# Optimization experiments

Hardware: AMD Instinct MI355X
Metric: run time of the kernel (lower is better)

## Reference

```python
import jax, jax.numpy as jnp
import numpy as np

N, K, M, C, OUT, S = 80000, 8, 1000, 128, 64, 2
EPS = 1e-5


def _bn(x, g, b, m, v):
    # eval-mode BatchNorm1d applied over the last (channel) axis
    return (x - m) * (g / jnp.sqrt(v + EPS)) + b


def setup_inputs() -> dict:
    key = jax.random.key(0)
    ks = jax.random.split(key, 40)
    it = iter(range(40))
    rn = lambda sh, s=1.0: jax.random.normal(ks[next(it)], sh, dtype=jnp.float32) * s
    ru = lambda sh: jax.random.uniform(ks[next(it)], sh, dtype=jnp.float32, minval=0.5, maxval=1.5)
    w = 0.05
    inp = {}
    inp["sp_fea"] = rn((M, C))
    inp["sp_xyz"] = rn((M, 3))
    inp["o_p_fea"] = rn((N, C))
    inp["p_xyz"] = rn((N, 3))
    # linear_q / linear_k / linear_v  (in_planes -> mid_planes)
    inp["Wq"] = rn((C, C), w); inp["bq"] = jnp.zeros((C,), jnp.float32)
    inp["Wk"] = rn((C, C), w); inp["bk"] = jnp.zeros((C,), jnp.float32)
    inp["Wv"] = rn((C, C), w); inp["bv"] = jnp.zeros((C,), jnp.float32)
    # linear_p: Linear(3,3) -> BN(3) -> ReLU -> Linear(3, mid)
    inp["Wp1"] = rn((3, 3), 0.5); inp["bp1"] = jnp.zeros((3,), jnp.float32)
    inp["gp"] = 1.0 + rn((3,), 0.1); inp["betap"] = rn((3,), 0.1)
    inp["mp"] = rn((3,), 0.1); inp["vp"] = ru((3,))
    inp["Wp2"] = rn((3, C), 0.3); inp["bp2"] = jnp.zeros((C,), jnp.float32)
    # linear_w: BN(mid) -> ReLU -> Linear(mid,out) -> BN(out) -> ReLU -> Linear(out,out)
    inp["g1"] = 1.0 + rn((C,), 0.1); inp["beta1"] = rn((C,), 0.1)
    inp["m1"] = rn((C,), 0.1); inp["v1"] = ru((C,))
    inp["W1"] = rn((C, OUT), w); inp["b1"] = jnp.zeros((OUT,), jnp.float32)
    inp["g2"] = 1.0 + rn((OUT,), 0.1); inp["beta2"] = rn((OUT,), 0.1)
    inp["m2"] = rn((OUT,), 0.1); inp["v2"] = ru((OUT,))
    inp["W2"] = rn((OUT, OUT), w); inp["b2"] = jnp.zeros((OUT,), jnp.float32)
    # index / offset inputs (ints)
    inp["c2p_idx_abs"] = jax.random.randint(ks[next(it)], (N, K), 0, M)
    inp["c2p_idx"] = jax.random.randint(ks[next(it)], (N, K), 0, M)
    inp["cluster_idx"] = jax.random.randint(ks[next(it)], (N,), 0, M)
    inp["offset"] = jnp.array([N], dtype=jnp.int32)
    inp["sp_offset"] = jnp.array([M], dtype=jnp.int32)
    return inp


def reference(sp_fea, sp_xyz, o_p_fea, p_xyz,
              Wq, bq, Wk, bk, Wv, bv,
              Wp1, bp1, gp, betap, mp, vp, Wp2, bp2,
              g1, beta1, m1, v1, W1, b1,
              g2, beta2, m2, v2, W2, b2,
              c2p_idx_abs, c2p_idx, cluster_idx, offset, sp_offset):
    q = o_p_fea @ Wq + bq                               # [N, C]
    k_sp = (sp_fea @ Wk + bk)[c2p_idx_abs]              # gather -> [N, K, C]
    v_sp = (sp_fea @ Wv + bv)[c2p_idx_abs]              # [N, K, C]
    p_e = sp_xyz[c2p_idx_abs]                           # [N, K, 3]
    # positional encoding MLP
    p_e = jax.nn.relu(_bn(p_e @ Wp1 + bp1, gp, betap, mp, vp)) @ Wp2 + bp2  # [N, K, C]
    # vector attention scores
    w = k_sp - q[:, None, :] + p_e                      # [N, K, C]
    w = jax.nn.relu(_bn(w, g1, beta1, m1, v1)) @ W1 + b1
    w = jax.nn.relu(_bn(w, g2, beta2, m2, v2)) @ W2 + b2  # [N, K, OUT]
    w = jax.nn.softmax(w, axis=1)                        # softmax over the K neighbors
    # shared-plane weighted sum
    bi = ((v_sp + p_e).reshape(N, K, S, C // S) * w[:, :, None, :]).reshape(N, K, C)
    bi = bi.sum(axis=2)                                  # [N, K]
    return jax.nn.softmax(bi, axis=1)                    # association matrix [N, K]
```

## Files before the change

kernel.cpp:

```cpp
#include <hip/hip_runtime.h>
#include <stdint.h>

#define EPS 1e-5f

#define NPTS 80000
#define CDIM 128
#define ODIM 64
#define KNBR 8
#define MSUP 1000

#define KP2H_OFF 0
#define UT_OFF   (256*1024)
#define WQF_OFF  (512*1024)
#define W1F_OFF  (544*1024)
#define W2F_OFF  (560*1024)
#define C1_OFF   (568*1024)
#define QSG_OFF  (576*1024)
#define WSTAGE_BYTES (16*1024 + 8*1024 + 256)

typedef float f32x4 __attribute__((ext_vector_type(4)));
typedef short bf16x8 __attribute__((ext_vector_type(8)));

union FragU { bf16x8 v; unsigned u[4]; uint4 q; };

#if __has_builtin(__builtin_amdgcn_cvt_pk_bf16_f32)
typedef __bf16 bf16x2_t __attribute__((ext_vector_type(2)));
#define HAVE_PK_BF16 1
#endif

__device__ inline unsigned pk_bf16(float lo, float hi) {
#ifdef HAVE_PK_BF16
  return __builtin_bit_cast(unsigned, __builtin_amdgcn_cvt_pk_bf16_f32(lo, hi));
#else
  unsigned a = __builtin_bit_cast(unsigned, lo);
  unsigned b = __builtin_bit_cast(unsigned, hi);
  a += 0x7FFFu + ((a >> 16) & 1u);
  b += 0x7FFFu + ((b >> 16) & 1u);
  return (a >> 16) | (b & 0xFFFF0000u);
#endif
}

__device__ inline void unpk(unsigned p, float& lo, float& hi) {
  lo = __builtin_bit_cast(float, p << 16);
  hi = __builtin_bit_cast(float, p & 0xFFFF0000u);
}

__global__ __launch_bounds__(256)
void k_prep(const float* __restrict__ sp_fea, const float* __restrict__ sp_xyz,
            const float* __restrict__ Wk, const float* __restrict__ bk,
            const float* __restrict__ Wv, const float* __restrict__ bv,
            const float* __restrict__ Wp1, const float* __restrict__ bp1,
            const float* __restrict__ gp, const float* __restrict__ betap,
            const float* __restrict__ mp, const float* __restrict__ vp,
            const float* __restrict__ Wp2, const float* __restrict__ bp2,
            const float* __restrict__ g1, const float* __restrict__ beta1,
            const float* __restrict__ m1, const float* __restrict__ v1,
            const float* __restrict__ bq,
            const float* __restrict__ Wq, const float* __restrict__ W1,
            const float* __restrict__ W2,
            const float* __restrict__ g2, const float* __restrict__ v2,
            const float* __restrict__ b1, const float* __restrict__ m2,
            const float* __restrict__ beta2, char* __restrict__ ws)
{
  if (blockIdx.x < 1000) {
    unsigned short* kp2h = (unsigned short*)(ws + KP2H_OFF);
    float* uT = (float*)(ws + UT_OFF);
    const int m = blockIdx.x;
    const int t = threadIdx.x;
    const int c = t & 127, half = t >> 7;
    __shared__ float fea[128];
    __shared__ float pk[128], pv[128];
    if (t < 128) fea[t] = sp_fea[m * 128 + t];
    __syncthreads();
    float kv = 0.f, vv = 0.f;
    const float* wkc = Wk + half * 64 * 128 + c;
    const float* wvc = Wv + half * 64 * 128 + c;
    const float* feah = fea + half * 64;
    #pragma unroll 8
    for (int d = 0; d < 64; ++d) {
      const float f = feah[d];
      kv = fmaf(f, wkc[d * 128], kv);
      vv = fmaf(f, wvc[d * 128], vv);
    }
    if (half) { pk[c] = kv; pv[c] = vv; }
    __syncthreads();
    if (!half) {
      kv += pk[c] + bk[c];
      vv += pv[c] + bv[c];
      const float x0 = sp_xyz[m*3+0], x1 = sp_xyz[m*3+1], x2 = sp_xyz[m*3+2];
      float pe = bp2[c];
      #pragma unroll
      for (int ii = 0; ii < 3; ++ii) {
        float s = bp1[ii] + x0*Wp1[0*3+ii] + x1*Wp1[1*3+ii] + x2*Wp1[2*3+ii];
        s = (s - mp[ii]) * (gp[ii] * rsqrtf(vp[ii] + EPS)) + betap[ii];
        s = fmaxf(s, 0.0f);
        pe += s * Wp2[ii*128 + c];
      }
      const float s1c = g1[c] * rsqrtf(v1[c] + EPS);
      const float kpv = (kv + pe - m1[c] - bq[c]) * s1c + beta1[c];
      kp2h[m*128 + c] = (unsigned short)(pk_bf16(kpv, kpv) & 0xFFFFu);
      pv[c] = vv + pe;
    }
    __syncthreads();
    if (t < 64) uT[m*64 + t] = pv[t] + pv[t + 64];
  } else {
    const int tid = (blockIdx.x - 1000) * 256 + threadIdx.x;
    if (tid < 2048) {
      const int e = tid, f = e >> 6, l = e & 63;
      const int kt = f >> 3, mt = f & 7;
      const int c = mt*16 + (l & 15);
      const int d0 = kt*32 + (l >> 4)*8;
      const float sc = g1[c] * rsqrtf(v1[c] + EPS);
      uint4 u;
      u.x = pk_bf16(Wq[(d0+0)*128 + c]*sc, Wq[(d0+1)*128 + c]*sc);
      u.y = pk_bf16(Wq[(d0+2)*128 + c]*sc, Wq[(d0+3)*128 + c]*sc);
      u.z = pk_bf16(Wq[(d0+4)*128 + c]*sc, Wq[(d0+5)*128 + c]*sc);
      u.w = pk_bf16(Wq[(d0+6)*128 + c]*sc, Wq[(d0+7)*128 + c]*sc);
      *(uint4*)(ws + WQF_OFF + e*16) = u;
    } else if (tid < 3072) {
      const int e = tid - 2048, f = e >> 6, l = e & 63;
      const int kt = f >> 2, jt = f & 3;
      const int j = jt*16 + (l & 15);
      const int c0 = kt*32 + (l >> 4)*8;
      const float sc = g2[j] * rsqrtf(v2[j] + EPS);
      uint4 u;
      u.x = pk_bf16(W1[(c0+0)*64 + j]*sc, W1[(c0+1)*64 + j]*sc);
      u.y = pk_bf16(W1[(c0+2)*64 + j]*sc, W1[(c0+3)*64 + j]*sc);
      u.z = pk_bf16(W1[(c0+4)*64 + j]*sc, W1[(c0+5)*64 + j]*sc);
      u.w = pk_bf16(W1[(c0+6)*64 + j]*sc, W1[(c0+7)*64 + j]*sc);
      *(uint4*)(ws + W1F_OFF + e*16) = u;
    } else if (tid < 3584) {
      const int e = tid - 3072, f = e >> 6, l = e & 63;
      const int kt2 = f >> 2, nt = f & 3;
      const int jp = nt*16 + (l & 15);
      const int j0 = kt2*32 + (l >> 4)*8;
      uint4 u;
      u.x = pk_bf16(W2[(j0+0)*64 + jp], W2[(j0+1)*64 + jp]);
      u.y = pk_bf16(W2[(j0+2)*64 + jp], W2[(j0+3)*64 + jp]);
      u.z = pk_bf16(W2[(j0+4)*64 + jp], W2[(j0+5)*64 + jp]);
      u.w = pk_bf16(W2[(j0+6)*64 + jp], W2[(j0+7)*64 + jp]);
      *(uint4*)(ws + W2F_OFF + e*16) = u;
    } else if (tid < 3648) {
      const int j = tid - 3584;
      const float sc = g2[j] * rsqrtf(v2[j] + EPS);
      ((float*)(ws + C1_OFF))[j] = (b1[j] - m2[j]) * sc + beta2[j];
    }
  }
}

__global__ __launch_bounds__(256, 4)
void k_q(const float* __restrict__ o_p_fea, char* __restrict__ ws)
{
  const bf16x8* wqf = (const bf16x8*)(ws + WQF_OFF);
  char* qs_g = ws + QSG_OFF;
  const int t = threadIdx.x;
  const int wave = t >> 6, l = t & 63;
  const int quad = l >> 4, row = l & 15;
  const int n0 = (blockIdx.x * 4 + wave) * 16;

  f32x4 qa[8];
  #pragma unroll
  for (int mt = 0; mt < 8; ++mt) qa[mt] = (f32x4){0.f, 0.f, 0.f, 0.f};
  const float* feab = o_p_fea + (size_t)(n0 + row) * 128;
  #pragma unroll
  for (int kt = 0; kt < 4; ++kt) {
    f32x4 fa = *(const f32x4*)(feab + kt*32 + quad*8);
    f32x4 fb = *(const f32x4*)(feab + kt*32 + quad*8 + 4);
    FragU bu;
    bu.u[0] = pk_bf16(fa[0], fa[1]);
    bu.u[1] = pk_bf16(fa[2], fa[3]);
    bu.u[2] = pk_bf16(fb[0], fb[1]);
    bu.u[3] = pk_bf16(fb[2], fb[3]);
    #pragma unroll
    for (int mt = 0; mt < 8; ++mt)
      qa[mt] = __builtin_amdgcn_mfma_f32_16x16x32_bf16(wqf[(kt*8+mt)*64 + l], bu.v, qa[mt], 0, 0, 0);
  }
  #pragma unroll
  for (int mt = 0; mt < 8; ++mt) {
    uint2 pp;
    pp.x = pk_bf16(qa[mt][0], qa[mt][1]);
    pp.y = pk_bf16(qa[mt][2], qa[mt][3]);
    *(uint2*)(qs_g + (size_t)(n0 + row) * 256 + mt*32 + quad*8) = pp;
  }
}

#define H2_PITCH 144
#define H2_SIZE  (16*144)
#define W1L_OFF  0
#define W2L_OFF  (16*1024)
#define C1L_OFF  (24*1024)
#define H2_BASE  24832
#define LDS_TOTAL (H2_BASE + 4*H2_SIZE)

__global__ __launch_bounds__(256, 3)
void k_main(const int* __restrict__ idx, const float* __restrict__ b2,
            const char* __restrict__ ws, float* __restrict__ out)
{
  const unsigned short* kp2h = (const unsigned short*)(ws + KP2H_OFF);
  const float* uT = (const float*)(ws + UT_OFF);
  const char* qs_g = ws + QSG_OFF;

  __shared__ __align__(16) char lds[LDS_TOTAL];
  const int t = threadIdx.x;
  const int wave = t >> 6, l = t & 63;
  const int quad = l >> 4, row = l & 15;
  char* h2_w = lds + H2_BASE + wave * H2_SIZE;

  const int sg = blockIdx.x * 4 + wave;
  const int n0 = sg * 16;
  const int idx_base = n0 * 8;
  const int nloc = row >> 3;

  {
    const uint4* src = (const uint4*)(ws + W1F_OFF);
    uint4* dst = (uint4*)lds;
    #pragma unroll
    for (int i = 0; i < 7; ++i) {
      const int e = t + i * 256;
      if (e < WSTAGE_BYTES / 16) dst[e] = src[e];
    }
  }

  int mr8[8];
  #pragma unroll
  for (int g = 0; g < 8; ++g) mr8[g] = idx[idx_base + g*16 + row];

  __syncthreads();

  f32x4 c1r[4];
  #pragma unroll
  for (int jt = 0; jt < 4; ++jt)
    c1r[jt] = *(const f32x4*)(lds + C1L_OFF + (jt*16 + quad*4)*4);
  float b2r[4];
  #pragma unroll
  for (int nt = 0; nt < 4; ++nt) b2r[nt] = b2[row + nt*16];

  int msc[4];
  #pragma unroll
  for (int rg = 0; rg < 4; ++rg) msc[rg] = idx[idx_base + quad*4 + rg];
  uint4 kfc[4], qpc[4];
  {
    const uint4* kr = (const uint4*)(kp2h + (size_t)mr8[0] * 128);
    const uint4* qr = (const uint4*)(qs_g + (size_t)(n0 + nloc) * 256);
    #pragma unroll
    for (int kt = 0; kt < 4; ++kt) { kfc[kt] = kr[kt*4 + quad]; qpc[kt] = qr[kt*4 + quad]; }
  }

  #pragma unroll 1
  for (int g = 0; g < 8; ++g) {
    int msn[4];
    uint4 kfn[4], qpn[4];
    if (g < 7) {
      #pragma unroll
      for (int rg = 0; rg < 4; ++rg) msn[rg] = idx[idx_base + (g+1)*16 + quad*4 + rg];
      const uint4* kr = (const uint4*)(kp2h + (size_t)mr8[g+1] * 128);
      const uint4* qr = (const uint4*)(qs_g + (size_t)(n0 + (g+1)*2 + nloc) * 256);
      #pragma unroll
      for (int kt = 0; kt < 4; ++kt) { kfn[kt] = kr[kt*4 + quad]; qpn[kt] = qr[kt*4 + quad]; }
    }
    float u4[4][4];
    #pragma unroll
    for (int rg = 0; rg < 4; ++rg) {
      const float* ur = uT + (size_t)msc[rg] * 64 + row;
      #pragma unroll
      for (int nt = 0; nt < 4; ++nt) u4[rg][nt] = ur[nt*16];
    }

    f32x4 a1[4];
    #pragma unroll
    for (int jt = 0; jt < 4; ++jt) a1[jt] = (f32x4){0.f, 0.f, 0.f, 0.f};
    #pragma unroll
    for (int kt = 0; kt < 4; ++kt) {
      const uint4 kp = kfc[kt];
      const uint4 qp = qpc[kt];
      FragU xf;
      {
        float klo, khi, qlo, qhi;
        unpk(kp.x, klo, khi); unpk(qp.x, qlo, qhi);
        xf.u[0] = pk_bf16(fmaxf(klo - qlo, 0.f), fmaxf(khi - qhi, 0.f));
        unpk(kp.y, klo, khi); unpk(qp.y, qlo, qhi);
        xf.u[1] = pk_bf16(fmaxf(klo - qlo, 0.f), fmaxf(khi - qhi, 0.f));
        unpk(kp.z, klo, khi); unpk(qp.z, qlo, qhi);
        xf.u[2] = pk_bf16(fmaxf(klo - qlo, 0.f), fmaxf(khi - qhi, 0.f));
        unpk(kp.w, klo, khi); unpk(qp.w, qlo, qhi);
        xf.u[3] = pk_bf16(fmaxf(klo - qlo, 0.f), fmaxf(khi - qhi, 0.f));
      }
      #pragma unroll
      for (int jt = 0; jt < 4; ++jt) {
        const bf16x8 wf = *(const bf16x8*)(lds + W1L_OFF + (kt*4+jt)*1024 + l*16);
        a1[jt] = __builtin_amdgcn_mfma_f32_16x16x32_bf16(wf, xf.v, a1[jt], 0, 0, 0);
      }
    }

    #pragma unroll
    for (int jt = 0; jt < 4; ++jt) {
      f32x4 v = a1[jt] + c1r[jt];
      uint2 pp;
      pp.x = pk_bf16(fmaxf(v[0], 0.f), fmaxf(v[1], 0.f));
      pp.y = pk_bf16(fmaxf(v[2], 0.f), fmaxf(v[3], 0.f));
      *(uint2*)(h2_w + row*H2_PITCH + (jt*16 + quad*4)*2) = pp;
    }

    f32x4 a2[4];
    #pragma unroll
    for (int nt = 0; nt < 4; ++nt) a2[nt] = (f32x4){0.f, 0.f, 0.f, 0.f};
    #pragma unroll
    for (int kt2 = 0; kt2 < 2; ++kt2) {
      const bf16x8 af = *(const bf16x8*)(h2_w + row*H2_PITCH + kt2*64 + quad*16);
      #pragma unroll
      for (int nt = 0; nt < 4; ++nt) {
        const bf16x8 wf = *(const bf16x8*)(lds + W2L_OFF + (kt2*4+nt)*1024 + l*16);
        a2[nt] = __builtin_amdgcn_mfma_f32_16x16x32_bf16(af, wf, a2[nt], 0, 0, 0);
      }
    }
    float e[4][4], rs[4];
    #pragma unroll
    for (int nt = 0; nt < 4; ++nt) {
      #pragma unroll
      for (int rg = 0; rg < 4; ++rg) e[nt][rg] = __expf(a2[nt][rg] + b2r[nt]);
      float s = e[nt][0] + e[nt][1] + e[nt][2] + e[nt][3];
      s += __shfl_xor(s, 16);
      rs[nt] = __builtin_amdgcn_rcpf(s);
    }
    float bi[4] = {0.f, 0.f, 0.f, 0.f};
    #pragma unroll
    for (int rg = 0; rg < 4; ++rg) {
      #pragma unroll
      for (int nt = 0; nt < 4; ++nt)
        bi[rg] = fmaf(e[nt][rg] * rs[nt], u4[rg][nt], bi[rg]);
    }
    #pragma unroll
    for (int rg = 0; rg < 4; ++rg) {
      float b = bi[rg];
      b += __shfl_xor(b, 1);
      b += __shfl_xor(b, 2);
      b += __shfl_xor(b, 4);
      b += __shfl_xor(b, 8);
      bi[rg] = b;
    }
    const float eb0 = __expf(bi[0]), eb1 = __expf(bi[1]);
    const float eb2 = __expf(bi[2]), eb3 = __expf(bi[3]);
    float sb = eb0 + eb1 + eb2 + eb3;
    sb += __shfl_xor(sb, 16);
    const float rsb = __builtin_amdgcn_rcpf(sb);
    if (row < 4) {
      const float vsel = row == 0 ? eb0 : row == 1 ? eb1 : row == 2 ? eb2 : eb3;
      out[n0*8 + g*16 + quad*4 + row] = vsel * rsb;
    }
    if (g < 7) {
      #pragma unroll
      for (int rg = 0; rg < 4; ++rg) msc[rg] = msn[rg];
      #pragma unroll
      for (int kt = 0; kt < 4; ++kt) { kfc[kt] = kfn[kt]; qpc[kt] = qpn[kt]; }
    }
  }
}

extern "C" void kernel_launch(void* const* d_in, const int* in_sizes, int n_in,
                              void* d_out, int out_size, void* d_ws, size_t ws_size,
                              hipStream_t stream)
{
  const float* sp_fea  = (const float*)d_in[0];
  const float* sp_xyz  = (const float*)d_in[1];
  const float* o_p_fea = (const float*)d_in[2];
  const float* Wq    = (const float*)d_in[4];
  const float* bq    = (const float*)d_in[5];
  const float* Wk    = (const float*)d_in[6];
  const float* bk    = (const float*)d_in[7];
  const float* Wv    = (const float*)d_in[8];
  const float* bv    = (const float*)d_in[9];
  const float* Wp1   = (const float*)d_in[10];
  const float* bp1   = (const float*)d_in[11];
  const float* gp    = (const float*)d_in[12];
  const float* betap = (const float*)d_in[13];
  const float* mp    = (const float*)d_in[14];
  const float* vp    = (const float*)d_in[15];
  const float* Wp2   = (const float*)d_in[16];
  const float* bp2   = (const float*)d_in[17];
  const float* g1    = (const float*)d_in[18];
  const float* beta1 = (const float*)d_in[19];
  const float* m1    = (const float*)d_in[20];
  const float* v1    = (const float*)d_in[21];
  const float* W1    = (const float*)d_in[22];
  const float* b1    = (const float*)d_in[23];
  const float* g2    = (const float*)d_in[24];
  const float* beta2 = (const float*)d_in[25];
  const float* m2    = (const float*)d_in[26];
  const float* v2    = (const float*)d_in[27];
  const float* W2    = (const float*)d_in[28];
  const float* b2    = (const float*)d_in[29];
  const int* c2p_idx_abs = (const int*)d_in[30];

  char* ws = (char*)d_ws;
  float* out = (float*)d_out;

  hipLaunchKernelGGL(k_prep, dim3(1015), dim3(256), 0, stream,
                     sp_fea, sp_xyz, Wk, bk, Wv, bv, Wp1, bp1, gp, betap, mp, vp,
                     Wp2, bp2, g1, beta1, m1, v1, bq,
                     Wq, W1, W2, g2, v2, b1, m2, beta2, ws);
  hipLaunchKernelGGL(k_q, dim3(1250), dim3(256), 0, stream,
                     o_p_fea, ws);
  hipLaunchKernelGGL(k_main, dim3(1250), dim3(256), 0, stream,
                     c2p_idx_abs, b2, ws, out);
}
```

Before: 221.5 us.

## Software-pipeline softmax epilogue one group behind MFMA and use packed bf16 ops

The exp/softmax/weighted-sum epilogue for each group now runs one iteration late, after the next group's MFMAs have been issued, so the transcendental and shuffle work can overlap matrix work. The separate unpack-to-fp32, subtract, relu and repack steps are replaced with native bf16 vector subtract and max, and the relu after layer 1 is done on packed bf16. Launch bounds go from 3 to 4 blocks per CU. The carried epilogue state adds register pressure against the tighter occupancy target, and subtracting in bf16 instead of fp32 changes rounding slightly.

Measured after the change: 414.5 us. 87.1% more time.

```diff
diff --git a/kernel.cpp b/kernel.cpp
--- a/kernel.cpp
+++ b/kernel.cpp
@@ -20,16 +20,18 @@
 
 typedef float f32x4 __attribute__((ext_vector_type(4)));
 typedef short bf16x8 __attribute__((ext_vector_type(8)));
+typedef __bf16 bf16v8 __attribute__((ext_vector_type(8)));
+typedef __bf16 bf16v4 __attribute__((ext_vector_type(4)));
 
 union FragU { bf16x8 v; unsigned u[4]; uint4 q; };
 
 #if __has_builtin(__builtin_amdgcn_cvt_pk_bf16_f32)
-typedef __bf16 bf16x2_t __attribute__((ext_vector_type(2)));
 #define HAVE_PK_BF16 1
 #endif
 
 __device__ inline unsigned pk_bf16(float lo, float hi) {
 #ifdef HAVE_PK_BF16
+  typedef __bf16 bf16x2_t __attribute__((ext_vector_type(2)));
   return __builtin_bit_cast(unsigned, __builtin_amdgcn_cvt_pk_bf16_f32(lo, hi));
 #else
   unsigned a = __builtin_bit_cast(unsigned, lo);
@@ -38,11 +40,6 @@
   b += 0x7FFFu + ((b >> 16) & 1u);
   return (a >> 16) | (b & 0xFFFF0000u);
 #endif
-}
-
-__device__ inline void unpk(unsigned p, float& lo, float& hi) {
-  lo = __builtin_bit_cast(float, p << 16);
-  hi = __builtin_bit_cast(float, p & 0xFFFF0000u);
 }
 
 __global__ __launch_bounds__(256)
@@ -192,7 +189,50 @@
 #define H2_BASE  24832
 #define LDS_TOTAL (H2_BASE + 4*H2_SIZE)
 
-__global__ __launch_bounds__(256, 3)
+struct EpiState { f32x4 a2[4]; float u4[4][4]; };
+
+__device__ __forceinline__ void epilogue(const EpiState& st, const float* b2r,
+                                         int quad, int row,
+                                         float* __restrict__ out, int base,
+                                         bool wr)
+{
+  float e[4][4], rs[4];
+  #pragma unroll
+  for (int nt = 0; nt < 4; ++nt) {
+    #pragma unroll
+    for (int rg = 0; rg < 4; ++rg) e[nt][rg] = __expf(st.a2[nt][rg] + b2r[nt]);
+    float s = e[nt][0] + e[nt][1] + e[nt][2] + e[nt][3];
+    s += __shfl_xor(s, 16);
+    rs[nt] = __builtin_amdgcn_rcpf(s);
+  }
+  float bi[4] = {0.f, 0.f, 0.f, 0.f};
+  #pragma unroll
+  for (int rg = 0; rg < 4; ++rg) {
+    #pragma unroll
+    for (int nt = 0; nt < 4; ++nt)
+      bi[rg] = fmaf(e[nt][rg] * rs[nt], st.u4[rg][nt], bi[rg]);
+  }
+  #pragma unroll
+  for (int rg = 0; rg < 4; ++rg) {
+    float b = bi[rg];
+    b += __shfl_xor(b, 1);
+    b += __shfl_xor(b, 2);
+    b += __shfl_xor(b, 4);
+    b += __shfl_xor(b, 8);
+    bi[rg] = b;
+  }
+  const float eb0 = __expf(bi[0]), eb1 = __expf(bi[1]);
+  const float eb2 = __expf(bi[2]), eb3 = __expf(bi[3]);
+  float sb = eb0 + eb1 + eb2 + eb3;
+  sb += __shfl_xor(sb, 16);
+  const float rsb = __builtin_amdgcn_rcpf(sb);
+  if (wr && row < 4) {
+    const float vsel = row == 0 ? eb0 : row == 1 ? eb1 : row == 2 ? eb2 : eb3;
+    out[base + quad*4 + row] = vsel * rsb;
+  }
+}
+
+__global__ __launch_bounds__(256, 4)
 void k_main(const int* __restrict__ idx, const float* __restrict__ b2,
             const char* __restrict__ ws, float* __restrict__ out)
 {
@@ -246,6 +286,14 @@
     for (int kt = 0; kt < 4; ++kt) { kfc[kt] = kr[kt*4 + quad]; qpc[kt] = qr[kt*4 + quad]; }
   }
 
+  EpiState st;
+  #pragma unroll
+  for (int nt = 0; nt < 4; ++nt) {
+    st.a2[nt] = (f32x4){0.f, 0.f, 0.f, 0.f};
+    #pragma unroll
+    for (int rg = 0; rg < 4; ++rg) st.u4[nt][rg] = 0.f;
+  }
+
   #pragma unroll 1
   for (int g = 0; g < 8; ++g) {
     int msn[4];
@@ -258,12 +306,12 @@
       #pragma unroll
       for (int kt = 0; kt < 4; ++kt) { kfn[kt] = kr[kt*4 + quad]; qpn[kt] = qr[kt*4 + quad]; }
     }
-    float u4[4][4];
+    float u4n[4][4];
     #pragma unroll
     for (int rg = 0; rg < 4; ++rg) {
       const float* ur = uT + (size_t)msc[rg] * 64 + row;
       #pragma unroll
-      for (int nt = 0; nt < 4; ++nt) u4[rg][nt] = ur[nt*16];
+      for (int nt = 0; nt < 4; ++nt) u4n[rg][nt] = ur[nt*16];
     }
 
     f32x4 a1[4];
@@ -271,20 +319,12 @@
     for (int jt = 0; jt < 4; ++jt) a1[jt] = (f32x4){0.f, 0.f, 0.f, 0.f};
     #pragma unroll
     for (int kt = 0; kt < 4; ++kt) {
-      const uint4 kp = kfc[kt];
-      const uint4 qp = qpc[kt];
+      const bf16v8 kv = __builtin_bit_cast(bf16v8, kfc[kt]);
+      const bf16v8 qv = __builtin_bit_cast(bf16v8, qpc[kt]);
+      bf16v8 z = {};
+      bf16v8 x = __builtin_elementwise_max((bf16v8)(kv - qv), z);
       FragU xf;
-      {
-        float klo, khi, qlo, qhi;
-        unpk(kp.x, klo, khi); unpk(qp.x, qlo, qhi);
-        xf.u[0] = pk_bf16(fmaxf(klo - qlo, 0.f), fmaxf(khi - qhi, 0.f));
-        unpk(kp.y, klo, khi); unpk(qp.y, qlo, qhi);
-        xf.u[1] = pk_bf16(fmaxf(klo - qlo, 0.f), fmaxf(khi - qhi, 0.f));
-        unpk(kp.z, klo, khi); unpk(qp.z, qlo, qhi);
-        xf.u[2] = pk_bf16(fmaxf(klo - qlo, 0.f), fmaxf(khi - qhi, 0.f));
-        unpk(kp.w, klo, khi); unpk(qp.w, qlo, qhi);
-        xf.u[3] = pk_bf16(fmaxf(klo - qlo, 0.f), fmaxf(khi - qhi, 0.f));
-      }
+      xf.q = __builtin_bit_cast(uint4, x);
       #pragma unroll
       for (int jt = 0; jt < 4; ++jt) {
         const bf16x8 wf = *(const bf16x8*)(lds + W1L_OFF + (kt*4+jt)*1024 + l*16);
@@ -296,8 +336,12 @@
     for (int jt = 0; jt < 4; ++jt) {
       f32x4 v = a1[jt] + c1r[jt];
       uint2 pp;
-      pp.x = pk_bf16(fmaxf(v[0], 0.f), fmaxf(v[1], 0.f));
-      pp.y = pk_bf16(fmaxf(v[2], 0.f), fmaxf(v[3], 0.f));
+      pp.x = pk_bf16(v[0], v[1]);
+      pp.y = pk_bf16(v[2], v[3]);
+      bf16v4 h = __builtin_bit_cast(bf16v4, pp);
+      bf16v4 z4 = {};
+      h = __builtin_elementwise_max(h, z4);
+      pp = __builtin_bit_cast(uint2, h);
       *(uint2*)(h2_w + row*H2_PITCH + (jt*16 + quad*4)*2) = pp;
     }
 
@@ -313,40 +357,19 @@
         a2[nt] = __builtin_amdgcn_mfma_f32_16x16x32_bf16(af, wf, a2[nt], 0, 0, 0);
       }
     }
-    float e[4][4], rs[4];
-    #pragma unroll
-    for (int nt = 0; nt < 4; ++nt) {
-      #pragma unroll
-      for (int rg = 0; rg < 4; ++rg) e[nt][rg] = __expf(a2[nt][rg] + b2r[nt]);
-      float s = e[nt][0] + e[nt][1] + e[nt][2] + e[nt][3];
-      s += __shfl_xor(s, 16);
-      rs[nt] = __builtin_amdgcn_rcpf(s);
-    }
-    float bi[4] = {0.f, 0.f, 0.f, 0.f};
-    #pragma unroll
-    for (int rg = 0; rg < 4; ++rg) {
-      #pragma unroll
-      for (int nt = 0; nt < 4; ++nt)
-        bi[rg] = fmaf(e[nt][rg] * rs[nt], u4[rg][nt], bi[rg]);
-    }
-    #pragma unroll
-    for (int rg = 0; rg < 4; ++rg) {
-      float b = bi[rg];
-      b += __shfl_xor(b, 1);
-      b += __shfl_xor(b, 2);
-      b += __shfl_xor(b, 4);
-      b += __shfl_xor(b, 8);
-      bi[rg] = b;
-    }
-    const float eb0 = __expf(bi[0]), eb1 = __expf(bi[1]);
-    const float eb2 = __expf(bi[2]), eb3 = __expf(bi[3]);
-    float sb = eb0 + eb1 + eb2 + eb3;
-    sb += __shfl_xor(sb, 16);
-    const float rsb = __builtin_amdgcn_rcpf(sb);
-    if (row < 4) {
-      const float vsel = row == 0 ? eb0 : row == 1 ? eb1 : row == 2 ? eb2 : eb3;
-      out[n0*8 + g*16 + quad*4 + row] = vsel * rsb;
-    }
+
+    {
+      const int gm1 = g - 1;
+      const int base = n0*8 + (gm1 < 0 ? 0 : gm1)*16;
+      epilogue(st, b2r, quad, row, out, base, gm1 >= 0);
+    }
+
+    #pragma unroll
+    for (int nt = 0; nt < 4; ++nt) st.a2[nt] = a2[nt];
+    #pragma unroll
+    for (int rg = 0; rg < 4; ++rg)
+      #pragma unroll
+      for (int nt = 0; nt < 4; ++nt) st.u4[rg][nt] = u4n[rg][nt];
     if (g < 7) {
       #pragma unroll
       for (int rg = 0; rg < 4; ++rg) msc[rg] = msn[rg];
@@ -354,6 +377,7 @@
       for (int kt = 0; kt < 4; ++kt) { kfc[kt] = kfn[kt]; qpc[kt] = qpn[kt]; }
     }
   }
+  epilogue(st, b2r, quad, row, out, n0*8 + 7*16, true);
 }
 
 extern "C" void kernel_launch(void* const* d_in, const int* in_sizes, int n_in,
```

## Stage Wq fragments in LDS and use packed bf16 subtract/max ops

Applied to the files above, without the earlier changes.

The q-projection kernel now copies the 32KB pre-fragmented Wq block into shared memory once per workgroup and reads MFMA A-fragments from LDS instead of global memory. In the main attention kernel, the k-q subtraction and ReLU are done directly on bf16 vectors instead of unpacking to fp32 and repacking, and the post-GEMM ReLU is applied after packing to bf16. The goal is fewer global loads and fewer ALU conversion instructions. In exchange it adds 32KB LDS per block in k_q, which can lower occupancy, and doing the subtraction in bf16 rounds differently. Packed bf16 arithmetic may also not map to native instructions, in which case the compiler expands it.

New measurement: 213.7 us. 1.04x faster.

```diff
diff --git a/kernel.cpp b/kernel.cpp
--- a/kernel.cpp
+++ b/kernel.cpp
@@ -20,16 +20,18 @@
 
 typedef float f32x4 __attribute__((ext_vector_type(4)));
 typedef short bf16x8 __attribute__((ext_vector_type(8)));
+typedef __bf16 bf16v8 __attribute__((ext_vector_type(8)));
+typedef __bf16 bf16v4 __attribute__((ext_vector_type(4)));
 
 union FragU { bf16x8 v; unsigned u[4]; uint4 q; };
 
 #if __has_builtin(__builtin_amdgcn_cvt_pk_bf16_f32)
-typedef __bf16 bf16x2_t __attribute__((ext_vector_type(2)));
 #define HAVE_PK_BF16 1
 #endif
 
 __device__ inline unsigned pk_bf16(float lo, float hi) {
 #ifdef HAVE_PK_BF16
+  typedef __bf16 bf16x2_t __attribute__((ext_vector_type(2)));
   return __builtin_bit_cast(unsigned, __builtin_amdgcn_cvt_pk_bf16_f32(lo, hi));
 #else
   unsigned a = __builtin_bit_cast(unsigned, lo);
@@ -38,11 +40,6 @@
   b += 0x7FFFu + ((b >> 16) & 1u);
   return (a >> 16) | (b & 0xFFFF0000u);
 #endif
-}
-
-__device__ inline void unpk(unsigned p, float& lo, float& hi) {
-  lo = __builtin_bit_cast(float, p << 16);
-  hi = __builtin_bit_cast(float, p & 0xFFFF0000u);
 }
 
 __global__ __launch_bounds__(256)
@@ -151,12 +148,20 @@
 __global__ __launch_bounds__(256, 4)
 void k_q(const float* __restrict__ o_p_fea, char* __restrict__ ws)
 {
-  const bf16x8* wqf = (const bf16x8*)(ws + WQF_OFF);
+  __shared__ __align__(16) char ldsq[32*1024];
   char* qs_g = ws + QSG_OFF;
   const int t = threadIdx.x;
   const int wave = t >> 6, l = t & 63;
   const int quad = l >> 4, row = l & 15;
   const int n0 = (blockIdx.x * 4 + wave) * 16;
+
+  {
+    const uint4* src = (const uint4*)(ws + WQF_OFF);
+    uint4* dst = (uint4*)ldsq;
+    #pragma unroll
+    for (int i = 0; i < 8; ++i) dst[t + i*256] = src[t + i*256];
+  }
+  __syncthreads();
 
   f32x4 qa[8];
   #pragma unroll
@@ -172,8 +177,10 @@
     bu.u[2] = pk_bf16(fb[0], fb[1]);
     bu.u[3] = pk_bf16(fb[2], fb[3]);
     #pragma unroll
-    for (int mt = 0; mt < 8; ++mt)
-      qa[mt] = __builtin_amdgcn_mfma_f32_16x16x32_bf16(wqf[(kt*8+mt)*64 + l], bu.v, qa[mt], 0, 0, 0);
+    for (int mt = 0; mt < 8; ++mt) {
+      const bf16x8 wf = *(const bf16x8*)(ldsq + ((kt*8+mt)*64 + l)*16);
+      qa[mt] = __builtin_amdgcn_mfma_f32_16x16x32_bf16(wf, bu.v, qa[mt], 0, 0, 0);
+    }
   }
   #pragma unroll
   for (int mt = 0; mt < 8; ++mt) {
@@ -271,20 +278,12 @@
     for (int jt = 0; jt < 4; ++jt) a1[jt] = (f32x4){0.f, 0.f, 0.f, 0.f};
     #pragma unroll
     for (int kt = 0; kt < 4; ++kt) {
-      const uint4 kp = kfc[kt];
-      const uint4 qp = qpc[kt];
+      const bf16v8 kv = __builtin_bit_cast(bf16v8, kfc[kt]);
+      const bf16v8 qv = __builtin_bit_cast(bf16v8, qpc[kt]);
+      bf16v8 z = {};
+      bf16v8 x = __builtin_elementwise_max((bf16v8)(kv - qv), z);
       FragU xf;
-      {
-        float klo, khi, qlo, qhi;
-        unpk(kp.x, klo, khi); unpk(qp.x, qlo, qhi);
-        xf.u[0] = pk_bf16(fmaxf(klo - qlo, 0.f), fmaxf(khi - qhi, 0.f));
-        unpk(kp.y, klo, khi); unpk(qp.y, qlo, qhi);
-        xf.u[1] = pk_bf16(fmaxf(klo - qlo, 0.f), fmaxf(khi - qhi, 0.f));
-        unpk(kp.z, klo, khi); unpk(qp.z, qlo, qhi);
-        xf.u[2] = pk_bf16(fmaxf(klo - qlo, 0.f), fmaxf(khi - qhi, 0.f));
-        unpk(kp.w, klo, khi); unpk(qp.w, qlo, qhi);
-        xf.u[3] = pk_bf16(fmaxf(klo - qlo, 0.f), fmaxf(khi - qhi, 0.f));
-      }
+      xf.q = __builtin_bit_cast(uint4, x);
       #pragma unroll
       for (int jt = 0; jt < 4; ++jt) {
         const bf16x8 wf = *(const bf16x8*)(lds + W1L_OFF + (kt*4+jt)*1024 + l*16);
@@ -296,8 +295,12 @@
     for (int jt = 0; jt < 4; ++jt) {
       f32x4 v = a1[jt] + c1r[jt];
       uint2 pp;
-      pp.x = pk_bf16(fmaxf(v[0], 0.f), fmaxf(v[1], 0.f));
-      pp.y = pk_bf16(fmaxf(v[2], 0.f), fmaxf(v[3], 0.f));
+      pp.x = pk_bf16(v[0], v[1]);
+      pp.y = pk_bf16(v[2], v[3]);
+      bf16v4 h = __builtin_bit_cast(bf16v4, pp);
+      bf16v4 z4 = {};
+      h = __builtin_elementwise_max(h, z4);
+      pp = __builtin_bit_cast(uint2, h);
       *(uint2*)(h2_w + row*H2_PITCH + (jt*16 + quad*4)*2) = pp;
     }
 
```
